# Kernel tuning notes

Hardware: AMD Instinct MI355X
Metric: run time of the kernel (lower is better)

The kernel has to match this reference:

```python
import jax, jax.numpy as jnp
import numpy as np

B, D, H, W = 32, 96, 96, 96
MAX_POINTS = 512
NUM_CLASSES = 512
# e3nn spherical-harmonic 'integral' normalization constants
C0 = 0.28209479177387814   # 1/(2*sqrt(pi))
C1 = 0.4886025119029199    # sqrt(3/(4*pi))
C2 = 0.6307831305050401    # sqrt(5/(4*pi))
SQ3 = 1.7320508075688772

# (multiplicity, irrep dim) blocks for each irreps layout
BLOCKS_IN = [(16, 1), (8, 3), (4, 5)]   # 16x0e + 8x1o + 4x2e = 60
BLOCKS_H1 = [(32, 1), (8, 3), (4, 5)]   # 76
BLOCKS_H2 = [(64, 1), (4, 3), (2, 5)]   # 86


def setup_inputs() -> dict:
    key = jax.random.key(0)
    ks = jax.random.split(key, 12)
    n = jax.random.normal
    return {
        "x": jax.random.uniform(ks[0], (B, 1, D, H, W), dtype=jnp.float32),
        "W1_0e": n(ks[1], (16, 32)), "W1_1o": n(ks[2], (8, 8)), "W1_2e": n(ks[3], (4, 4)),
        "W2_0e": n(ks[4], (32, 64)), "W2_1o": n(ks[5], (8, 4)), "W2_2e": n(ks[6], (4, 2)),
        "W3_0e": n(ks[7], (64, 128)),
        "fc1_w": n(ks[8], (128, 64)) * 0.05, "fc1_b": jnp.zeros((64,), jnp.float32),
        "fc2_w": n(ks[9], (64, NUM_CLASSES)) * 0.05, "fc2_b": jnp.zeros((NUM_CLASSES,), jnp.float32),
    }


def _topk_pointcloud(x):
    # topk sampling path: highest-density voxels (threshold filter is a no-op
    # for top-k when enough voxels pass, which holds here). x: (B,1,D,H,W)
    vol = x[:, 0]
    flat = vol.reshape(vol.shape[0], -1)
    vals, idx = jax.lax.top_k(flat, MAX_POINTS)          # (B,N)
    z = idx // (H * W)
    rem = idx % (H * W)
    y = rem // W
    xw = rem % W
    coords = jnp.stack([z, y, xw], axis=-1).astype(jnp.float32)  # (B,N,3)
    center = jnp.array([D, H, W], jnp.float32) / 2.0
    scale = float(max(D, H, W)) / 2.0
    points = (coords - center) / scale
    return points, vals


def _point_features(pts, vals):
    # pts: (B,N,3) normalized coords, vals: (B,N) densities -> (B,N,60)
    v = vals[..., None]
    denom = vals.sum(axis=1, keepdims=True)
    com = (pts * v).sum(axis=1) / jnp.maximum(denom, 1e-12)      # (B,3)
    c = pts - com[:, None, :]
    r = jnp.maximum(jnp.linalg.norm(c, axis=-1), 1e-6)           # r_safe (B,N)
    rr = r[..., None]
    d = c / rr                                                   # unit directions
    dx, dy, dz = d[..., 0], d[..., 1], d[..., 2]
    sh1 = C1 * d                                                 # l=1 SH, e3nn order (x,y,z)
    sh2 = C2 * jnp.stack([
        SQ3 * dx * dz,
        SQ3 * dx * dy,
        dy * dy - 0.5 * (dx * dx + dz * dz),
        SQ3 * dy * dz,
        0.5 * SQ3 * (dz * dz - dx * dx),
    ], axis=-1)                                                  # (B,N,5)
    l1pr = jnp.log1p(r)
    sh0 = jnp.full_like(vals, C0)
    scalars = jnp.stack([
        vals, r, sh0, vals * r, vals ** 2, l1pr, jnp.sqrt(vals + 1e-6),
        r ** 2, vals * sh0, jnp.exp(-r), vals ** 3, jnp.sqrt(r),
        vals * l1pr, jax.nn.sigmoid(vals), jax.nn.sigmoid(r), vals * r ** 2,
    ], axis=-1)                                                  # (B,N,16)
    vectors = jnp.concatenate([
        c, c * v, sh1, c * rr, d, d * v, c * v ** 2, sh1 * rr,
    ], axis=-1)                                                  # (B,N,24)
    tensors = jnp.concatenate([
        sh2, sh2 * v, sh2 * rr, sh2 * l1pr[..., None],
    ], axis=-1)                                                  # (B,N,20)
    return jnp.concatenate([scalars, vectors, tensors], axis=-1)


def _irreps_linear(feat, blocks, weights):
    # e3nn o3.Linear: block-diagonal per-irrep linear, one path per block,
    # path normalization 1/sqrt(mul_in). Blocks laid out mul-major.
    outs = []
    start = 0
    for (mul_in, dim), Wb in zip(blocks, weights):
        blk = feat[..., start:start + mul_in * dim]
        blk = blk.reshape(*feat.shape[:-1], mul_in, dim)
        out = jnp.einsum('bnui,uv->bnvi', blk, Wb) / np.sqrt(mul_in).astype(np.float32)
        outs.append(out.reshape(*feat.shape[:-1], -1))
        start += mul_in * dim
    return jnp.concatenate(outs, axis=-1)


def reference(x, W1_0e, W1_1o, W1_2e, W2_0e, W2_1o, W2_2e, W3_0e,
              fc1_w, fc1_b, fc2_w, fc2_b):
    pts, vals = _topk_pointcloud(x)
    feat = _point_features(pts, vals)                    # (B,512,60)
    h = _irreps_linear(feat, BLOCKS_IN, [W1_0e, W1_1o, W1_2e])   # (B,512,76)
    h = _irreps_linear(h, BLOCKS_H1, [W2_0e, W2_1o, W2_2e])      # (B,512,86)
    # layer3 -> 128x0e: only the 0e path exists, 1o/2e inputs are dropped
    h = _irreps_linear(h[..., :64], [(64, 1)], [W3_0e])          # (B,512,128)
    pooled = h.max(axis=1)                               # (B,128)
    hid = jax.nn.relu(pooled @ fc1_w + fc1_b)            # dropout is eval-mode identity
    logits = hid @ fc2_w + fc2_b
    return logits, feat
```

## Files before the change

### kernel.cpp

```cpp
#include <hip/hip_runtime.h>
#include <hip/hip_bf16.h>
#include <stdint.h>

#define NVOX   884736
#define NB     32
#define NPTS   512
#define CAP    4096
#define THRV   0.9990234375f
#define THR_TOP 0x3F7FFFFFu
#define BPB    216
#define SLOT   64
#define LBUF   80
#define NBUCK  128

#define C0c  0.28209479177387814f
#define C1c  0.4886025119029199f
#define C2c  0.6307831305050401f
#define SQ3c 1.7320508075688772f

typedef unsigned long long u64;
typedef unsigned int u32;

__global__ __launch_bounds__(256) void k_collect(const float* __restrict__ x,
                                                 u64* __restrict__ cand,
                                                 u32* __restrict__ counts,
                                                 const float* __restrict__ W1,
                                                 const float* __restrict__ W2,
                                                 const float* __restrict__ W3,
                                                 float* __restrict__ Mg) {
  const int b   = blockIdx.y;
  const int blk = blockIdx.x;
  const int tid = threadIdx.x;
  __shared__ u64 lbuf[LBUF];
  __shared__ float Tm[16 * 64];
  __shared__ int lcnt;
  if (tid == 0) lcnt = 0;
  __syncthreads();

  const float4* xb = reinterpret_cast<const float4*>(x + (size_t)b * NVOX);
  const int t0 = blk * 1024 + tid;
  float4 q[4];
  #pragma unroll
  for (int it = 0; it < 4; ++it) q[it] = xb[t0 + it * 256];

  #pragma unroll
  for (int it = 0; it < 4; ++it) {
    const float4 qq = q[it];
    const u32 base = (u32)(t0 + it * 256) * 4u;
    if (qq.x >= THRV) { int p = atomicAdd(&lcnt, 1); if (p < LBUF) lbuf[p] = ((u64)__float_as_uint(qq.x) << 32) | (u64)(~(base      )); }
    if (qq.y >= THRV) { int p = atomicAdd(&lcnt, 1); if (p < LBUF) lbuf[p] = ((u64)__float_as_uint(qq.y) << 32) | (u64)(~(base + 1u)); }
    if (qq.z >= THRV) { int p = atomicAdd(&lcnt, 1); if (p < LBUF) lbuf[p] = ((u64)__float_as_uint(qq.z) << 32) | (u64)(~(base + 2u)); }
    if (qq.w >= THRV) { int p = atomicAdd(&lcnt, 1); if (p < LBUF) lbuf[p] = ((u64)__float_as_uint(qq.w) << 32) | (u64)(~(base + 3u)); }
  }
  __syncthreads();

  const int slot = b * BPB + blk;
  const int n = lcnt;
  const int wn = (n <= SLOT) ? n : SLOT;
  if (tid < wn) cand[(size_t)slot * SLOT + tid] = lbuf[tid];
  if (tid == 0) counts[slot] = (n <= SLOT) ? (u32)n : (u32)(SLOT + 1);

  if (blk == 0 && b == 0) {
    const float s1c = 1.0f / (4.0f * sqrtf(32.0f));
    for (int e = tid; e < 16 * 64; e += 256) {
      const int u = e >> 6, j = e & 63;
      float s = 0.f;
      for (int k = 0; k < 32; ++k) s += W1[u * 32 + k] * W2[k * 64 + j];
      Tm[e] = s * s1c;
    }
    __syncthreads();
    for (int e = tid; e < 16 * 128; e += 256) {
      const int u = e >> 7, vv = e & 127;
      float s = 0.f;
      for (int j = 0; j < 64; ++j) s += Tm[u * 64 + j] * W3[j * 128 + vv];
      Mg[e] = s * 0.125f;
    }
  }
}

__global__ __launch_bounds__(512) void k_select(const float* __restrict__ x,
                                                const u64* __restrict__ cand,
                                                const u32* __restrict__ counts,
                                                u64* __restrict__ sel,
                                                float* __restrict__ comvg) {
  const int b   = blockIdx.x;
  const int tid = threadIdx.x;

  __shared__ u64 lk[CAP];
  __shared__ u64 lk2[CAP];
  __shared__ u64 sk[NPTS];
  __shared__ u32 sA[256], sB[256];
  __shared__ u32 scnt[BPB], spref[BPB];
  __shared__ u32 bc[NBUCK], bbx[NBUCK], bp[NBUCK], bA[NBUCK], bB[NBUCK];
  __shared__ float rbuf[8][4];
  __shared__ int sbad, sC;
  __shared__ u32 sthr;

  u32 myc = 0;
  if (tid == 0) sbad = 0;
  if (tid < 256) { myc = (tid < BPB) ? counts[b * BPB + tid] : 0u; sA[tid] = myc; }
  __syncthreads();
  if (tid < BPB && myc > SLOT) atomicOr(&sbad, 1);
  u32 *ssrc = sA, *sdst = sB;
  for (int off = 1; off < 256; off <<= 1) {
    if (tid < 256) sdst[tid] = ssrc[tid] + ((tid >= off) ? ssrc[tid - off] : 0u);
    __syncthreads();
    u32* t = ssrc; ssrc = sdst; sdst = t;
  }
  const int total = (int)ssrc[255];
  if (tid < BPB) { scnt[tid] = myc; spref[tid] = ssrc[tid] - myc; }
  __syncthreads();

  int C;
  if (!sbad && total >= NPTS && total <= CAP) {
    C = total;
    for (int s = tid >> 1; s < BPB; s += 256) {
      const u32 c = scnt[s], p = spref[s];
      const u64* src = cand + (size_t)(b * BPB + s) * SLOT;
      for (u32 k = (u32)(tid & 1); k < c; k += 2) lk[p + k] = src[k];
    }
    __syncthreads();
  } else {
    u32* hist = reinterpret_cast<u32*>(lk);
    for (int i = tid; i < 4096; i += 512) hist[i] = 0u;
    __syncthreads();
    const u32* xb = reinterpret_cast<const u32*>(x) + (size_t)b * NVOX;
    for (int i = tid; i < NVOX; i += 512) {
      const u32 bits = xb[i];
      u32 key;
      if (bits >= 0x3F800000u) key = 0u;
      else { const u32 dd = THR_TOP - bits; key = dd >> 8; if (key > 4095u) key = 4095u; }
      atomicAdd(&hist[key], 1u);
    }
    __syncthreads();
    if (tid == 0) {
      u32 cum = 0; int kt = 4095;
      for (int k = 0; k < 4096; ++k) { cum += hist[k]; if (cum >= (u32)NPTS) { kt = k; break; } }
      sthr = (kt >= 4095) ? 0u : (0x3F800000u - ((u32)(kt + 1) << 8));
      sC = 0;
    }
    __syncthreads();
    const u32 thr = sthr;
    for (int i = tid; i < NVOX; i += 512) {
      const u32 bits = xb[i];
      if (bits >= thr) {
        const int p = atomicAdd(&sC, 1);
        if (p < CAP) lk[p] = ((u64)bits << 32) | (u64)(~(u32)i);
      }
    }
    __syncthreads();
    C = sC < CAP ? sC : CAP;
    __syncthreads();
  }

  if (tid < NBUCK) bc[tid] = 0u;
  __syncthreads();
  for (int i = tid; i < C; i += 512) {
    const u32 bits = (u32)(lk[i] >> 32);
    u32 bk = (THR_TOP - bits) >> 7; if (bk > (NBUCK - 1)) bk = NBUCK - 1;
    atomicAdd(&bc[bk], 1u);
  }
  __syncthreads();
  if (tid < NBUCK) bA[tid] = bc[tid];
  __syncthreads();
  u32 *bsrc = bA, *bdst = bB;
  for (int off = 1; off < NBUCK; off <<= 1) {
    if (tid < NBUCK) bdst[tid] = bsrc[tid] + ((tid >= off) ? bsrc[tid - off] : 0u);
    __syncthreads();
    u32* t = bsrc; bsrc = bdst; bdst = t;
  }
  if (tid < NBUCK) { bbx[tid] = bsrc[tid] - bc[tid]; bp[tid] = bsrc[tid] - bc[tid]; }
  __syncthreads();
  for (int i = tid; i < C; i += 512) {
    const u64 ki = lk[i];
    const u32 bits = (u32)(ki >> 32);
    u32 bk = (THR_TOP - bits) >> 7; if (bk > (NBUCK - 1)) bk = NBUCK - 1;
    const u32 p = atomicAdd(&bp[bk], 1u);
    lk2[p] = ki;
  }
  __syncthreads();
  for (int i = tid; i < C; i += 512) {
    const u64 ki = lk2[i];
    const u32 bits = (u32)(ki >> 32);
    u32 bk = (THR_TOP - bits) >> 7; if (bk > (NBUCK - 1)) bk = NBUCK - 1;
    const u32 lo = bbx[bk], hi = lo + bc[bk];
    int rank = (int)lo;
    for (u32 j = lo; j < hi; ++j) rank += (lk2[j] > ki) ? 1 : 0;
    if (rank < NPTS) sk[rank] = ki;
  }
  __syncthreads();

  const u64 key = sk[tid];
  sel[(size_t)b * NPTS + tid] = key;

  const u32 bits = (u32)(key >> 32);
  const u32 idx  = ~((u32)key);
  const float v  = __uint_as_float(bits);
  const u32 z = idx / 9216u, rem = idx % 9216u, yy = rem / 96u, xw = rem % 96u;
  const float p0 = ((float)z  - 48.f) / 48.f;
  const float p1 = ((float)yy - 48.f) / 48.f;
  const float p2 = ((float)xw - 48.f) / 48.f;
  float sv = v, s0 = p0 * v, s1 = p1 * v, s2 = p2 * v;
  for (int off = 32; off > 0; off >>= 1) {
    sv += __shfl_down(sv, off);
    s0 += __shfl_down(s0, off);
    s1 += __shfl_down(s1, off);
    s2 += __shfl_down(s2, off);
  }
  const int w = tid >> 6, ln = tid & 63;
  if (ln == 0) { rbuf[w][0] = sv; rbuf[w][1] = s0; rbuf[w][2] = s1; rbuf[w][3] = s2; }
  __syncthreads();
  if (tid == 0) {
    float tv = 0.f, t0s = 0.f, t1s = 0.f, t2s = 0.f;
    for (int wv = 0; wv < 8; ++wv) { tv += rbuf[wv][0]; t0s += rbuf[wv][1]; t1s += rbuf[wv][2]; t2s += rbuf[wv][3]; }
    const float dnm = fmaxf(tv, 1e-12f);
    comvg[b * 4 + 0] = t0s / dnm; comvg[b * 4 + 1] = t1s / dnm;
    comvg[b * 4 + 2] = t2s / dnm; comvg[b * 4 + 3] = 0.f;
  }
}

__global__ __launch_bounds__(512) void k_featpool(const u64* __restrict__ sel,
                                                  const float* __restrict__ comvg,
                                                  const float* __restrict__ Mg,
                                                  float* __restrict__ ppart,
                                                  float* __restrict__ dout) {
  const int p8  = blockIdx.x;
  const int b   = blockIdx.y;
  const int tid = threadIdx.x;
  __shared__ float Ms[16 * 128];
  __shared__ __align__(16) float fs[64][20];
  __shared__ float pr[4][128];

  for (int e = tid; e < 16 * 128; e += 512) Ms[e] = Mg[e];

  const int pl = tid >> 3, cg = tid & 7;
  const int gp = b * NPTS + p8 * 64 + pl;
  const u64 key = sel[gp];
  const u32 bits = (u32)(key >> 32);
  const u32 idx  = ~((u32)key);
  const float v  = __uint_as_float(bits);
  const u32 z = idx / 9216u, rem = idx % 9216u, yy = rem / 96u, xw = rem % 96u;
  const float4 cm = reinterpret_cast<const float4*>(comvg)[b];
  const float c0 = ((float)z  - 48.f) / 48.f - cm.x;
  const float c1 = ((float)yy - 48.f) / 48.f - cm.y;
  const float c2 = ((float)xw - 48.f) / 48.f - cm.z;
  const float r = fmaxf(sqrtf(c0 * c0 + c1 * c1 + c2 * c2), 1e-6f);
  const float inv = 1.0f / r;
  const float d0 = c0 * inv, d1 = c1 * inv, d2 = c2 * inv;
  const float v2 = v * v;
  const float rr2 = r * r;
  const float l1 = log1pf(r);
  const float er = expf(-r);
  const float sgv = 1.0f / (1.0f + expf(-v));
  const float sgr = 1.0f / (1.0f + expf(-r));

  float f[60];
  f[0]=v;      f[1]=r;      f[2]=C0c;     f[3]=v*r;
  f[4]=v2;     f[5]=l1;     f[6]=sqrtf(v + 1e-6f); f[7]=rr2;
  f[8]=v*C0c;  f[9]=er;     f[10]=v2*v;   f[11]=sqrtf(r);
  f[12]=v*l1;  f[13]=sgv;   f[14]=sgr;    f[15]=v*rr2;
  f[16]=c0;        f[17]=c1;        f[18]=c2;
  f[19]=c0*v;      f[20]=c1*v;      f[21]=c2*v;
  f[22]=C1c*d0;    f[23]=C1c*d1;    f[24]=C1c*d2;
  f[25]=c0*r;      f[26]=c1*r;      f[27]=c2*r;
  f[28]=d0;        f[29]=d1;        f[30]=d2;
  f[31]=d0*v;      f[32]=d1*v;      f[33]=d2*v;
  f[34]=c0*v2;     f[35]=c1*v2;     f[36]=c2*v2;
  f[37]=C1c*d0*r;  f[38]=C1c*d1*r;  f[39]=C1c*d2*r;
  const float t0 = C2c * (SQ3c * d0 * d2);
  const float t1 = C2c * (SQ3c * d0 * d1);
  const float t2_ = C2c * (d1 * d1 - 0.5f * (d0 * d0 + d2 * d2));
  const float t3 = C2c * (SQ3c * d1 * d2);
  const float t4 = C2c * (0.5f * SQ3c * (d2 * d2 - d0 * d0));
  f[40]=t0;     f[41]=t1;     f[42]=t2_;     f[43]=t3;     f[44]=t4;
  f[45]=t0*v;   f[46]=t1*v;   f[47]=t2_*v;   f[48]=t3*v;   f[49]=t4*v;
  f[50]=t0*r;   f[51]=t1*r;   f[52]=t2_*r;   f[53]=t3*r;   f[54]=t4*r;
  f[55]=t0*l1;  f[56]=t1*l1;  f[57]=t2_*l1;  f[58]=t3*l1;  f[59]=t4*l1;

  float4* ob = reinterpret_cast<float4*>(dout + 16384 + (size_t)gp * 60);
  #pragma unroll
  for (int k = 0; k < 15; ++k)
    if ((k & 7) == cg) ob[k] = make_float4(f[4*k], f[4*k+1], f[4*k+2], f[4*k+3]);

  #pragma unroll
  for (int k = 0; k < 4; ++k)
    if (k == cg) *reinterpret_cast<float4*>(&fs[pl][k * 4]) =
        make_float4(f[4*k], f[4*k+1], f[4*k+2], f[4*k+3]);
  __syncthreads();

  const int g = tid >> 7, vv = tid & 127;
  float mreg[16];
  #pragma unroll
  for (int u = 0; u < 16; ++u) mreg[u] = Ms[u * 128 + vv];
  float pm = -3.4e38f;
  for (int n = g; n < 64; n += 4) {
    const float4 a0 = *reinterpret_cast<const float4*>(&fs[n][0]);
    const float4 a1 = *reinterpret_cast<const float4*>(&fs[n][4]);
    const float4 a2 = *reinterpret_cast<const float4*>(&fs[n][8]);
    const float4 a3 = *reinterpret_cast<const float4*>(&fs[n][12]);
    float acc = a0.x*mreg[0] + a0.y*mreg[1] + a0.z*mreg[2] + a0.w*mreg[3]
              + a1.x*mreg[4] + a1.y*mreg[5] + a1.z*mreg[6] + a1.w*mreg[7]
              + a2.x*mreg[8] + a2.y*mreg[9] + a2.z*mreg[10]+ a2.w*mreg[11]
              + a3.x*mreg[12]+ a3.y*mreg[13]+ a3.z*mreg[14]+ a3.w*mreg[15];
    pm = fmaxf(pm, acc);
  }
  pr[g][vv] = pm;
  __syncthreads();
  if (g == 0)
    ppart[((size_t)b * 8 + p8) * 128 + vv] =
        fmaxf(fmaxf(pr[0][vv], pr[1][vv]), fmaxf(pr[2][vv], pr[3][vv]));
}

__global__ __launch_bounds__(512) void k_head(const float* __restrict__ ppart,
                                              const float* __restrict__ fc1w,
                                              const float* __restrict__ fc1b,
                                              const float* __restrict__ fc2w,
                                              const float* __restrict__ fc2b,
                                              float* __restrict__ dout) {
  const int b = blockIdx.x;
  const int t = threadIdx.x;
  __shared__ float pl[128];
  __shared__ float hid[64];
  if (t < 128) {
    float m = -3.4e38f;
    #pragma unroll
    for (int k = 0; k < 8; ++k) m = fmaxf(m, ppart[((size_t)b * 8 + k) * 128 + t]);
    pl[t] = m;
  }
  __syncthreads();
  if (t < 64) {
    float sh = fc1b[t];
    for (int u = 0; u < 128; ++u) sh += pl[u] * fc1w[u * 64 + t];
    hid[t] = fmaxf(sh, 0.f);
  }
  __syncthreads();
  float sl = fc2b[t];
  for (int j = 0; j < 64; ++j) sl += hid[j] * fc2w[j * 512 + t];
  dout[b * 512 + t] = sl;
}

extern "C" void kernel_launch(void* const* d_in, const int* in_sizes, int n_in,
                              void* d_out, int out_size, void* d_ws, size_t ws_size,
                              hipStream_t stream) {
  const float* x    = (const float*)d_in[0];
  const float* W1   = (const float*)d_in[1];
  const float* W2   = (const float*)d_in[4];
  const float* W3   = (const float*)d_in[7];
  const float* fc1w = (const float*)d_in[8];
  const float* fc1b = (const float*)d_in[9];
  const float* fc2w = (const float*)d_in[10];
  const float* fc2b = (const float*)d_in[11];
  float* out = (float*)d_out;

  uint8_t* ws = (uint8_t*)d_ws;
  u32*   counts = (u32*)ws;
  u64*   cand   = (u64*)(ws + 0x10000);
  u64*   sel    = (u64*)(ws + 0x400000);
  float* comv   = (float*)(ws + 0x420000);
  float* ppart  = (float*)(ws + 0x421000);
  float* Mg     = (float*)(ws + 0x450000);

  dim3 g1(BPB, NB);
  k_collect<<<g1, 256, 0, stream>>>(x, cand, counts, W1, W2, W3, Mg);
  k_select<<<NB, 512, 0, stream>>>(x, cand, counts, sel, comv);
  dim3 g3(8, NB);
  k_featpool<<<g3, 512, 0, stream>>>(sel, comv, Mg, ppart, out);
  k_head<<<NB, 512, 0, stream>>>(ppart, fc1w, fc1b, fc2w, fc2b, out);
}
```

Before: 42.46 us.

## Fuse top-k selection with feature/pool kernel, recomputing selection per block

Merges k_select and k_featpool into one kernel launched on an 8x32 grid. Each of the 8 blocks per batch redoes the full candidate selection, sort and center-of-mass reduction, then computes features and the partial max-pool for its own 64-point slice. This removes one kernel launch and the global round trip for the selected keys and center of mass. In exchange the selection work is repeated eight times per batch, and the larger shared-memory footprint may lower occupancy.

After: 41.51 us. 1.02x faster.

```diff
diff --git a/kernel.cpp b/kernel.cpp
--- a/kernel.cpp
+++ b/kernel.cpp
@@ -78,12 +78,14 @@
   }
 }
 
-__global__ __launch_bounds__(512) void k_select(const float* __restrict__ x,
-                                                const u64* __restrict__ cand,
-                                                const u32* __restrict__ counts,
-                                                u64* __restrict__ sel,
-                                                float* __restrict__ comvg) {
-  const int b   = blockIdx.x;
+__global__ __launch_bounds__(512) void k_selfeat(const float* __restrict__ x,
+                                                 const u64* __restrict__ cand,
+                                                 const u32* __restrict__ counts,
+                                                 const float* __restrict__ Mg,
+                                                 float* __restrict__ ppart,
+                                                 float* __restrict__ dout) {
+  const int p8  = blockIdx.x;
+  const int b   = blockIdx.y;
   const int tid = threadIdx.x;
 
   __shared__ u64 lk[CAP];
@@ -93,8 +95,14 @@
   __shared__ u32 scnt[BPB], spref[BPB];
   __shared__ u32 bc[NBUCK], bbx[NBUCK], bp[NBUCK], bA[NBUCK], bB[NBUCK];
   __shared__ float rbuf[8][4];
+  __shared__ float comv[4];
+  __shared__ float Ms[16 * 128];
+  __shared__ __align__(16) float fsb[64][20];
+  __shared__ float pr[4][128];
   __shared__ int sbad, sC;
   __shared__ u32 sthr;
+
+  for (int e = tid; e < 16 * 128; e += 512) Ms[e] = Mg[e];
 
   u32 myc = 0;
   if (tid == 0) sbad = 0;
@@ -190,60 +198,44 @@
   }
   __syncthreads();
 
-  const u64 key = sk[tid];
-  sel[(size_t)b * NPTS + tid] = key;
-
+  {
+    const u64 key = sk[tid];
+    const u32 bits = (u32)(key >> 32);
+    const u32 idx  = ~((u32)key);
+    const float v  = __uint_as_float(bits);
+    const u32 z = idx / 9216u, rem = idx % 9216u, yy = rem / 96u, xw = rem % 96u;
+    const float p0 = ((float)z  - 48.f) / 48.f;
+    const float p1 = ((float)yy - 48.f) / 48.f;
+    const float p2 = ((float)xw - 48.f) / 48.f;
+    float sv = v, s0 = p0 * v, s1 = p1 * v, s2 = p2 * v;
+    for (int off = 32; off > 0; off >>= 1) {
+      sv += __shfl_down(sv, off);
+      s0 += __shfl_down(s0, off);
+      s1 += __shfl_down(s1, off);
+      s2 += __shfl_down(s2, off);
+    }
+    const int w = tid >> 6, ln = tid & 63;
+    if (ln == 0) { rbuf[w][0] = sv; rbuf[w][1] = s0; rbuf[w][2] = s1; rbuf[w][3] = s2; }
+    __syncthreads();
+    if (tid == 0) {
+      float tv = 0.f, t0s = 0.f, t1s = 0.f, t2s = 0.f;
+      for (int wv = 0; wv < 8; ++wv) { tv += rbuf[wv][0]; t0s += rbuf[wv][1]; t1s += rbuf[wv][2]; t2s += rbuf[wv][3]; }
+      const float dnm = fmaxf(tv, 1e-12f);
+      comv[0] = t0s / dnm; comv[1] = t1s / dnm; comv[2] = t2s / dnm;
+    }
+    __syncthreads();
+  }
+
+  const int pl = tid >> 3, cg = tid & 7;
+  const int gp = b * NPTS + p8 * 64 + pl;
+  const u64 key = sk[p8 * 64 + pl];
   const u32 bits = (u32)(key >> 32);
   const u32 idx  = ~((u32)key);
   const float v  = __uint_as_float(bits);
   const u32 z = idx / 9216u, rem = idx % 9216u, yy = rem / 96u, xw = rem % 96u;
-  const float p0 = ((float)z  - 48.f) / 48.f;
-  const float p1 = ((float)yy - 48.f) / 48.f;
-  const float p2 = ((float)xw - 48.f) / 48.f;
-  float sv = v, s0 = p0 * v, s1 = p1 * v, s2 = p2 * v;
-  for (int off = 32; off > 0; off >>= 1) {
-    sv += __shfl_down(sv, off);
-    s0 += __shfl_down(s0, off);
-    s1 += __shfl_down(s1, off);
-    s2 += __shfl_down(s2, off);
-  }
-  const int w = tid >> 6, ln = tid & 63;
-  if (ln == 0) { rbuf[w][0] = sv; rbuf[w][1] = s0; rbuf[w][2] = s1; rbuf[w][3] = s2; }
-  __syncthreads();
-  if (tid == 0) {
-    float tv = 0.f, t0s = 0.f, t1s = 0.f, t2s = 0.f;
-    for (int wv = 0; wv < 8; ++wv) { tv += rbuf[wv][0]; t0s += rbuf[wv][1]; t1s += rbuf[wv][2]; t2s += rbuf[wv][3]; }
-    const float dnm = fmaxf(tv, 1e-12f);
-    comvg[b * 4 + 0] = t0s / dnm; comvg[b * 4 + 1] = t1s / dnm;
-    comvg[b * 4 + 2] = t2s / dnm; comvg[b * 4 + 3] = 0.f;
-  }
-}
-
-__global__ __launch_bounds__(512) void k_featpool(const u64* __restrict__ sel,
-                                                  const float* __restrict__ comvg,
-                                                  const float* __restrict__ Mg,
-                                                  float* __restrict__ ppart,
-                                                  float* __restrict__ dout) {
-  const int p8  = blockIdx.x;
-  const int b   = blockIdx.y;
-  const int tid = threadIdx.x;
-  __shared__ float Ms[16 * 128];
-  __shared__ __align__(16) float fs[64][20];
-  __shared__ float pr[4][128];
-
-  for (int e = tid; e < 16 * 128; e += 512) Ms[e] = Mg[e];
-
-  const int pl = tid >> 3, cg = tid & 7;
-  const int gp = b * NPTS + p8 * 64 + pl;
-  const u64 key = sel[gp];
-  const u32 bits = (u32)(key >> 32);
-  const u32 idx  = ~((u32)key);
-  const float v  = __uint_as_float(bits);
-  const u32 z = idx / 9216u, rem = idx % 9216u, yy = rem / 96u, xw = rem % 96u;
-  const float4 cm = reinterpret_cast<const float4*>(comvg)[b];
-  const float c0 = ((float)z  - 48.f) / 48.f - cm.x;
-  const float c1 = ((float)yy - 48.f) / 48.f - cm.y;
-  const float c2 = ((float)xw - 48.f) / 48.f - cm.z;
+  const float c0 = ((float)z  - 48.f) / 48.f - comv[0];
+  const float c1 = ((float)yy - 48.f) / 48.f - comv[1];
+  const float c2 = ((float)xw - 48.f) / 48.f - comv[2];
   const float r = fmaxf(sqrtf(c0 * c0 + c1 * c1 + c2 * c2), 1e-6f);
   const float inv = 1.0f / r;
   const float d0 = c0 * inv, d1 = c1 * inv, d2 = c2 * inv;
@@ -284,7 +276,7 @@
 
   #pragma unroll
   for (int k = 0; k < 4; ++k)
-    if (k == cg) *reinterpret_cast<float4*>(&fs[pl][k * 4]) =
+    if (k == cg) *reinterpret_cast<float4*>(&fsb[pl][k * 4]) =
         make_float4(f[4*k], f[4*k+1], f[4*k+2], f[4*k+3]);
   __syncthreads();
 
@@ -294,10 +286,10 @@
   for (int u = 0; u < 16; ++u) mreg[u] = Ms[u * 128 + vv];
   float pm = -3.4e38f;
   for (int n = g; n < 64; n += 4) {
-    const float4 a0 = *reinterpret_cast<const float4*>(&fs[n][0]);
-    const float4 a1 = *reinterpret_cast<const float4*>(&fs[n][4]);
-    const float4 a2 = *reinterpret_cast<const float4*>(&fs[n][8]);
-    const float4 a3 = *reinterpret_cast<const float4*>(&fs[n][12]);
+    const float4 a0 = *reinterpret_cast<const float4*>(&fsb[n][0]);
+    const float4 a1 = *reinterpret_cast<const float4*>(&fsb[n][4]);
+    const float4 a2 = *reinterpret_cast<const float4*>(&fsb[n][8]);
+    const float4 a3 = *reinterpret_cast<const float4*>(&fsb[n][12]);
     float acc = a0.x*mreg[0] + a0.y*mreg[1] + a0.z*mreg[2] + a0.w*mreg[3]
               + a1.x*mreg[4] + a1.y*mreg[5] + a1.z*mreg[6] + a1.w*mreg[7]
               + a2.x*mreg[8] + a2.y*mreg[9] + a2.z*mreg[10]+ a2.w*mreg[11]
@@ -355,15 +347,12 @@
   uint8_t* ws = (uint8_t*)d_ws;
   u32*   counts = (u32*)ws;
   u64*   cand   = (u64*)(ws + 0x10000);
-  u64*   sel    = (u64*)(ws + 0x400000);
-  float* comv   = (float*)(ws + 0x420000);
-  float* ppart  = (float*)(ws + 0x421000);
-  float* Mg     = (float*)(ws + 0x450000);
+  float* ppart  = (float*)(ws + 0x3A0000);
+  float* Mg     = (float*)(ws + 0x3C0000);
 
   dim3 g1(BPB, NB);
   k_collect<<<g1, 256, 0, stream>>>(x, cand, counts, W1, W2, W3, Mg);
-  k_select<<<NB, 512, 0, stream>>>(x, cand, counts, sel, comv);
-  dim3 g3(8, NB);
-  k_featpool<<<g3, 512, 0, stream>>>(sel, comv, Mg, ppart, out);
+  dim3 g2(8, NB);
+  k_selfeat<<<g2, 512, 0, stream>>>(x, cand, counts, Mg, ppart, out);
   k_head<<<NB, 512, 0, stream>>>(ppart, fc1w, fc1b, fc2w, fc2b, out);
 }
```
